# Optimization experiments

Measured on AMD Instinct MI355X. Metric: run time of the kernel, lower is better.

## Reference

```python
import jax, jax.numpy as jnp
import numpy as np

NUM_EXPERTS = 128
INPUT_DIM = 128
HIDDEN_DIM = 512
OUTPUT_DIM = 128
TOKENS_PER_EXPERT = 2048


def make_identity_experts(num_experts, input_dim, output_dim):
    # identical to the torch helper: zeros with ones on the (square) diagonal
    d = min(input_dim, output_dim)
    w = jnp.zeros((num_experts, input_dim, output_dim), dtype=jnp.float32)
    idx = jnp.arange(d)
    return w.at[:, idx, idx].set(1.0)


def setup_inputs() -> dict:
    key = jax.random.key(0)
    k_tok, = jax.random.split(key, 1)
    group_token = jax.random.normal(
        k_tok, (NUM_EXPERTS, TOKENS_PER_EXPERT, INPUT_DIM), dtype=jnp.float32)
    weights1 = make_identity_experts(NUM_EXPERTS, INPUT_DIM, HIDDEN_DIM)
    weights2 = make_identity_experts(NUM_EXPERTS, HIDDEN_DIM, OUTPUT_DIM)
    return {"group_token": group_token, "weights1": weights1, "weights2": weights2}


def reference(group_token, weights1, weights2):
    # grouped GEMM 1: per-expert [T, in] @ [in, hid]
    h = jnp.einsum('etd,edh->eth', group_token, weights1)
    # exact (erf-based) GELU, matching torch.nn.functional.gelu default
    h = jax.nn.gelu(h, approximate=False)
    # grouped GEMM 2: per-expert [T, hid] @ [hid, out]
    out = jnp.einsum('eth,eho->eto', h, weights2)
    return out
```

## Files before the change

### kernel.cpp

```cpp
#include <hip/hip_runtime.h>
#include <hip/hip_bf16.h>
#include <stdint.h>

typedef __attribute__((ext_vector_type(8))) short s8v;
typedef __attribute__((ext_vector_type(4))) float f4v;

#define NE   128
#define NT   2048
#define DIN  128
#define DH   512
#define DOUT 128

#define MFMA32(a,b,c) __builtin_amdgcn_mfma_f32_16x16x32_bf16(a,b,c,0,0,0)

#define GLOAD16(g,l) __builtin_amdgcn_global_load_lds( \
    (const __attribute__((address_space(1))) void*)(g), \
    (__attribute__((address_space(3))) void*)(l), 16, 0, 0)

#define WAIT_VM(N) asm volatile("s_waitcnt vmcnt(" #N ")" ::: "memory")
#define BAR() do { asm volatile("" ::: "memory"); \
                   __builtin_amdgcn_s_barrier();  \
                   asm volatile("" ::: "memory"); } while (0)

__device__ __forceinline__ __hip_bfloat162 pk2(float a, float b) {
  float2 t; t.x = a; t.y = b;
  return __float22bfloat162_rn(t);
}

__device__ __forceinline__ s8v pack8(float4 a, float4 b) {
  union { s8v v; __hip_bfloat162 h[4]; } u;
  u.h[0] = pk2(a.x, a.y); u.h[1] = pk2(a.z, a.w);
  u.h[2] = pk2(b.x, b.y); u.h[3] = pk2(b.z, b.w);
  return u.v;
}

__device__ __forceinline__ float gelu_f(float x) {
  float x2 = x * x;
  float p  = __builtin_fmaf(x2, 0.07135481f, 1.5957691f);
  float e  = __expf(-x * p);
  return x * __builtin_amdgcn_rcpf(1.0f + e);
}

__device__ __forceinline__ float4 gelu4(f4v v) {
  float4 r;
  r.x = gelu_f(v[0]); r.y = gelu_f(v[1]);
  r.z = gelu_f(v[2]); r.w = gelu_f(v[3]);
  return r;
}

#define W1_BLOCKS (NE * 4)
#define W2_BLOCKS (NE * 16)
__global__ __launch_bounds__(256) void pack_weights(
    const float* __restrict__ W1, const float* __restrict__ W2,
    ushort* __restrict__ W1F, ushort* __restrict__ W2F) {
  __shared__ __align__(16) float T[32 * 132];
  const int tid = threadIdx.x;
  const int lane = tid & 63, wid = tid >> 6;
  const int q = lane >> 4, l16 = lane & 15;

  if ((int)blockIdx.x < W1_BLOCKS) {
    const int e = blockIdx.x >> 2, ks = blockIdx.x & 3;
    const float* We = W1 + (size_t)e * (DIN * DH) + (size_t)(ks * 32) * DH;
    const int r = tid >> 3, c0 = (tid & 7) * 16;
    for (int hc = 0; hc < 4; ++hc) {
      if (hc) __syncthreads();
      const float* src = We + (size_t)r * DH + hc * 128 + c0;
      float4 v0 = *(const float4*)(src + 0);
      float4 v1 = *(const float4*)(src + 4);
      float4 v2 = *(const float4*)(src + 8);
      float4 v3 = *(const float4*)(src + 12);
      float* t = &T[r * 132 + c0];
      *(float4*)(t + 0) = v0; *(float4*)(t + 4)  = v1;
      *(float4*)(t + 8) = v2; *(float4*)(t + 12) = v3;
      __syncthreads();
#pragma unroll
      for (int i = 0; i < 2; ++i) {
        const int htl = wid + 4 * i;
        const int ht  = hc * 8 + htl;
        float g[8];
#pragma unroll
        for (int j = 0; j < 8; ++j) g[j] = T[(8 * q + j) * 132 + 16 * htl + l16];
        float4 a; a.x = g[0]; a.y = g[1]; a.z = g[2]; a.w = g[3];
        float4 b; b.x = g[4]; b.y = g[5]; b.z = g[6]; b.w = g[7];
        *(s8v*)(W1F + ((((size_t)e * 32 + ht) * 4) + ks) * 512 + lane * 8) = pack8(a, b);
      }
    }
  } else {
    const int bb = (int)blockIdx.x - W1_BLOCKS;
    const int e = bb >> 4, ct = bb & 15;
    const int r = tid >> 3, c0 = (tid & 7) * 16;
    const float* src = W2 + (size_t)e * (DH * DOUT) + (size_t)(ct * 32 + r) * DOUT + c0;
    float4 v0 = *(const float4*)(src + 0);
    float4 v1 = *(const float4*)(src + 4);
    float4 v2 = *(const float4*)(src + 8);
    float4 v3 = *(const float4*)(src + 12);
    float* t = &T[r * 132 + c0];
    *(float4*)(t + 0) = v0; *(float4*)(t + 4)  = v1;
    *(float4*)(t + 8) = v2; *(float4*)(t + 12) = v3;
    __syncthreads();
#pragma unroll
    for (int i = 0; i < 2; ++i) {
      const int ot = wid + 4 * i;
      float g[8];
#pragma unroll
      for (int j = 0; j < 8; ++j) {
        const int sig = (j < 4) ? (4 * q + j) : (16 + 4 * q + (j - 4));
        g[j] = T[sig * 132 + ot * 16 + l16];
      }
      float4 a; a.x = g[0]; a.y = g[1]; a.z = g[2]; a.w = g[3];
      float4 b; b.x = g[4]; b.y = g[5]; b.z = g[6]; b.w = g[7];
      *(s8v*)(W2F + (((size_t)e * 16 + ct) * 8 + ot) * 512 + lane * 8) = pack8(a, b);
    }
  }
}

__global__ __launch_bounds__(256, 3) void moe_fused(
    const float* __restrict__ X, const ushort* __restrict__ W1F,
    const ushort* __restrict__ W2F, float* __restrict__ Out) {
  __shared__ __align__(16) ushort W1s[2][4096];
  __shared__ __align__(16) ushort W2s[2][4096];

  const int tid  = threadIdx.x;
  const int lane = tid & 63;
  const int wid  = tid >> 6;
  const int q    = lane >> 4;
  const int l16  = lane & 15;

  const int bid  = blockIdx.x;
  const int wk   = ((bid & 7) << 8) | (bid >> 3);
  const int e    = wk >> 4;
  const int tile = wk & 15;

  const float* Xe  = X + ((size_t)e * NT + (size_t)tile * 128) * DIN;
  const ushort* W1e = W1F + (size_t)e * 65536;
  const ushort* W2e = W2F + (size_t)e * 65536;
  float* Oe = Out + ((size_t)e * NT + (size_t)tile * 128) * DOUT;

  s8v xf[2][4];
#pragma unroll
  for (int mt = 0; mt < 2; ++mt) {
#pragma unroll
    for (int ks = 0; ks < 4; ++ks) {
      const float* p = Xe + (size_t)(wid * 32 + mt * 16 + l16) * DIN + ks * 32 + q * 8;
      float4 v0 = *(const float4*)p;
      float4 v1 = *(const float4*)(p + 4);
      xf[mt][ks] = pack8(v0, v1);
    }
  }

  const f4v zero4 = {0.0f, 0.0f, 0.0f, 0.0f};
  f4v oacc[2][8];
#pragma unroll
  for (int mt = 0; mt < 2; ++mt)
#pragma unroll
    for (int ot = 0; ot < 8; ++ot) oacc[mt][ot] = zero4;

  auto stage = [&](int chunk, int b) {
    const ushort* g1 = W1e + chunk * 4096;
    const ushort* g2 = W2e + chunk * 4096;
#pragma unroll
    for (int i = 0; i < 2; ++i) {
      int u = i * 256 + tid;
      GLOAD16(g1 + u * 8, &W1s[b][u * 8]);
      GLOAD16(g2 + u * 8, &W2s[b][u * 8]);
    }
  };

  asm volatile("" ::: "memory");

  stage(0, 0);

  for (int c = 0; c < 16; ++c) {
    const int buf = c & 1;
    WAIT_VM(0);
    BAR();
    if (c < 15) stage(c + 1, buf ^ 1);

    f4v h0[2]; h0[0] = zero4; h0[1] = zero4;
#pragma unroll
    for (int kp = 0; kp < 2; ++kp) {
      s8v af0 = *(const s8v*)&W1s[buf][(kp * 2 + 0) * 512 + lane * 8];
      s8v af1 = *(const s8v*)&W1s[buf][(kp * 2 + 1) * 512 + lane * 8];
      __builtin_amdgcn_s_setprio(1);
      h0[0] = MFMA32(af0, xf[0][kp * 2 + 0], h0[0]);
      h0[1] = MFMA32(af0, xf[1][kp * 2 + 0], h0[1]);
      h0[0] = MFMA32(af1, xf[0][kp * 2 + 1], h0[0]);
      h0[1] = MFMA32(af1, xf[1][kp * 2 + 1], h0[1]);
      __builtin_amdgcn_s_setprio(0);
    }
    float4 ga0 = gelu4(h0[0]);
    float4 ga1 = gelu4(h0[1]);

    f4v h1[2]; h1[0] = zero4; h1[1] = zero4;
#pragma unroll
    for (int kp = 0; kp < 2; ++kp) {
      s8v af0 = *(const s8v*)&W1s[buf][(4 + kp * 2 + 0) * 512 + lane * 8];
      s8v af1 = *(const s8v*)&W1s[buf][(4 + kp * 2 + 1) * 512 + lane * 8];
      __builtin_amdgcn_s_setprio(1);
      h1[0] = MFMA32(af0, xf[0][kp * 2 + 0], h1[0]);
      h1[1] = MFMA32(af0, xf[1][kp * 2 + 0], h1[1]);
      h1[0] = MFMA32(af1, xf[0][kp * 2 + 1], h1[0]);
      h1[1] = MFMA32(af1, xf[1][kp * 2 + 1], h1[1]);
      __builtin_amdgcn_s_setprio(0);
    }

    s8v a8_0 = pack8(ga0, gelu4(h1[0]));
    s8v a8_1 = pack8(ga1, gelu4(h1[1]));

#pragma unroll
    for (int op = 0; op < 4; ++op) {
      s8v b0 = *(const s8v*)&W2s[buf][(op * 2 + 0) * 512 + lane * 8];
      s8v b1 = *(const s8v*)&W2s[buf][(op * 2 + 1) * 512 + lane * 8];
      __builtin_amdgcn_s_setprio(1);
      oacc[0][op * 2 + 0] = MFMA32(a8_0, b0, oacc[0][op * 2 + 0]);
      oacc[1][op * 2 + 0] = MFMA32(a8_1, b0, oacc[1][op * 2 + 0]);
      oacc[0][op * 2 + 1] = MFMA32(a8_0, b1, oacc[0][op * 2 + 1]);
      oacc[1][op * 2 + 1] = MFMA32(a8_1, b1, oacc[1][op * 2 + 1]);
      __builtin_amdgcn_s_setprio(0);
    }
  }

#pragma unroll
  for (int mt = 0; mt < 2; ++mt) {
    const int mb = wid * 32 + mt * 16 + 4 * q;
#pragma unroll
    for (int ot = 0; ot < 8; ++ot) {
      float* p = Oe + (size_t)mb * DOUT + ot * 16 + l16;
      p[0 * DOUT] = oacc[mt][ot][0];
      p[1 * DOUT] = oacc[mt][ot][1];
      p[2 * DOUT] = oacc[mt][ot][2];
      p[3 * DOUT] = oacc[mt][ot][3];
    }
  }
}

extern "C" void kernel_launch(void* const* d_in, const int* in_sizes, int n_in,
                              void* d_out, int out_size, void* d_ws, size_t ws_size,
                              hipStream_t stream) {
  const float* X  = (const float*)d_in[0];
  const float* W1 = (const float*)d_in[1];
  const float* W2 = (const float*)d_in[2];
  float* Out = (float*)d_out;

  ushort* W1F = (ushort*)d_ws;
  ushort* W2F = (ushort*)d_ws + (size_t)NE * 65536;

  pack_weights<<<W1_BLOCKS + W2_BLOCKS, 256, 0, stream>>>(W1, W2, W1F, W2F);
  moe_fused<<<NE * (NT / 128), 256, 0, stream>>>(X, W1F, W2F, Out);
}
```

Before: 338.2 us.

## Load packed weight fragments directly from global memory instead of LDS staging

```diff
diff --git a/kernel.cpp b/kernel.cpp
--- a/kernel.cpp
+++ b/kernel.cpp
@@ -12,15 +12,6 @@
 #define DOUT 128
 
 #define MFMA32(a,b,c) __builtin_amdgcn_mfma_f32_16x16x32_bf16(a,b,c,0,0,0)
-
-#define GLOAD16(g,l) __builtin_amdgcn_global_load_lds( \
-    (const __attribute__((address_space(1))) void*)(g), \
-    (__attribute__((address_space(3))) void*)(l), 16, 0, 0)
-
-#define WAIT_VM(N) asm volatile("s_waitcnt vmcnt(" #N ")" ::: "memory")
-#define BAR() do { asm volatile("" ::: "memory"); \
-                   __builtin_amdgcn_s_barrier();  \
-                   asm volatile("" ::: "memory"); } while (0)
 
 __device__ __forceinline__ __hip_bfloat162 pk2(float a, float b) {
   float2 t; t.x = a; t.y = b;
@@ -117,9 +108,6 @@
 __global__ __launch_bounds__(256, 3) void moe_fused(
     const float* __restrict__ X, const ushort* __restrict__ W1F,
     const ushort* __restrict__ W2F, float* __restrict__ Out) {
-  __shared__ __align__(16) ushort W1s[2][4096];
-  __shared__ __align__(16) ushort W2s[2][4096];
-
   const int tid  = threadIdx.x;
   const int lane = tid & 63;
   const int wid  = tid >> 6;
@@ -132,8 +120,8 @@
   const int tile = wk & 15;
 
   const float* Xe  = X + ((size_t)e * NT + (size_t)tile * 128) * DIN;
-  const ushort* W1e = W1F + (size_t)e * 65536;
-  const ushort* W2e = W2F + (size_t)e * 65536;
+  const ushort* W1e = W1F + (size_t)e * 65536 + lane * 8;
+  const ushort* W2e = W2F + (size_t)e * 65536 + lane * 8;
   float* Oe = Out + ((size_t)e * NT + (size_t)tile * 128) * DOUT;
 
   s8v xf[2][4];
@@ -155,62 +143,42 @@
 #pragma unroll
     for (int ot = 0; ot < 8; ++ot) oacc[mt][ot] = zero4;
 
-  auto stage = [&](int chunk, int b) {
-    const ushort* g1 = W1e + chunk * 4096;
-    const ushort* g2 = W2e + chunk * 4096;
-#pragma unroll
-    for (int i = 0; i < 2; ++i) {
-      int u = i * 256 + tid;
-      GLOAD16(g1 + u * 8, &W1s[b][u * 8]);
-      GLOAD16(g2 + u * 8, &W2s[b][u * 8]);
-    }
-  };
-
-  asm volatile("" ::: "memory");
-
-  stage(0, 0);
-
+#pragma unroll 1
   for (int c = 0; c < 16; ++c) {
-    const int buf = c & 1;
-    WAIT_VM(0);
-    BAR();
-    if (c < 15) stage(c + 1, buf ^ 1);
+    const ushort* W1c = W1e + c * 4096;
+    const ushort* W2c = W2e + c * 4096;
+
+    s8v af[8];
+#pragma unroll
+    for (int k = 0; k < 8; ++k) af[k] = *(const s8v*)(W1c + k * 512);
 
     f4v h0[2]; h0[0] = zero4; h0[1] = zero4;
-#pragma unroll
-    for (int kp = 0; kp < 2; ++kp) {
-      s8v af0 = *(const s8v*)&W1s[buf][(kp * 2 + 0) * 512 + lane * 8];
-      s8v af1 = *(const s8v*)&W1s[buf][(kp * 2 + 1) * 512 + lane * 8];
-      __builtin_amdgcn_s_setprio(1);
-      h0[0] = MFMA32(af0, xf[0][kp * 2 + 0], h0[0]);
-      h0[1] = MFMA32(af0, xf[1][kp * 2 + 0], h0[1]);
-      h0[0] = MFMA32(af1, xf[0][kp * 2 + 1], h0[0]);
-      h0[1] = MFMA32(af1, xf[1][kp * 2 + 1], h0[1]);
-      __builtin_amdgcn_s_setprio(0);
-    }
+    __builtin_amdgcn_s_setprio(1);
+#pragma unroll
+    for (int ks = 0; ks < 4; ++ks) {
+      h0[0] = MFMA32(af[ks], xf[0][ks], h0[0]);
+      h0[1] = MFMA32(af[ks], xf[1][ks], h0[1]);
+    }
+    __builtin_amdgcn_s_setprio(0);
     float4 ga0 = gelu4(h0[0]);
     float4 ga1 = gelu4(h0[1]);
 
     f4v h1[2]; h1[0] = zero4; h1[1] = zero4;
-#pragma unroll
-    for (int kp = 0; kp < 2; ++kp) {
-      s8v af0 = *(const s8v*)&W1s[buf][(4 + kp * 2 + 0) * 512 + lane * 8];
-      s8v af1 = *(const s8v*)&W1s[buf][(4 + kp * 2 + 1) * 512 + lane * 8];
-      __builtin_amdgcn_s_setprio(1);
-      h1[0] = MFMA32(af0, xf[0][kp * 2 + 0], h1[0]);
-      h1[1] = MFMA32(af0, xf[1][kp * 2 + 0], h1[1]);
-      h1[0] = MFMA32(af1, xf[0][kp * 2 + 1], h1[0]);
-      h1[1] = MFMA32(af1, xf[1][kp * 2 + 1], h1[1]);
-      __builtin_amdgcn_s_setprio(0);
-    }
+    __builtin_amdgcn_s_setprio(1);
+#pragma unroll
+    for (int ks = 0; ks < 4; ++ks) {
+      h1[0] = MFMA32(af[4 + ks], xf[0][ks], h1[0]);
+      h1[1] = MFMA32(af[4 + ks], xf[1][ks], h1[1]);
+    }
+    __builtin_amdgcn_s_setprio(0);
 
     s8v a8_0 = pack8(ga0, gelu4(h1[0]));
     s8v a8_1 = pack8(ga1, gelu4(h1[1]));
 
 #pragma unroll
     for (int op = 0; op < 4; ++op) {
-      s8v b0 = *(const s8v*)&W2s[buf][(op * 2 + 0) * 512 + lane * 8];
-      s8v b1 = *(const s8v*)&W2s[buf][(op * 2 + 1) * 512 + lane * 8];
+      s8v b0 = *(const s8v*)(W2c + (op * 2 + 0) * 512);
+      s8v b1 = *(const s8v*)(W2c + (op * 2 + 1) * 512);
       __builtin_amdgcn_s_setprio(1);
       oacc[0][op * 2 + 0] = MFMA32(a8_0, b0, oacc[0][op * 2 + 0]);
       oacc[1][op * 2 + 0] = MFMA32(a8_1, b0, oacc[1][op * 2 + 0]);
```

New measurement: 373.9 us. +10.6%, slower.
